# Performance work log

Hardware: AMD Instinct MI355X
Metric: run time of the kernel (lower is better)

## Reference

```python
import jax, jax.numpy as jnp
import numpy as np

WINDOW = 20  # local attention window, per create_sparse_mask


def _make_mask(rng, n, sparsity_ratio=0.1):
    # local band: |i - j| <= window//2 (covers start/end clamping and the diagonal)
    idx = jnp.arange(n)
    mask = jnp.abs(idx[:, None] - idx[None, :]) <= (WINDOW // 2)
    # random edges: n_random (i, j) pairs set to 1 (duplicates harmless)
    n_random = int(sparsity_ratio * n * n)
    k1, k2 = jax.random.split(rng)
    ri = jax.random.randint(k1, (n_random,), 0, n)
    rj = jax.random.randint(k2, (n_random,), 0, n)
    mask = mask.at[ri, rj].set(True)
    return mask  # [n, n] bool


def setup_inputs() -> dict:
    rng = jax.random.key(0)
    kq, kk, kv, km = jax.random.split(rng, 4)
    B, H, S, D = 1, 8, 4096, 32
    return {
        "query": jax.random.normal(kq, (B, H, S, D), dtype=jnp.float32),
        "key": jax.random.normal(kk, (B, H, S, D), dtype=jnp.float32),
        "value": jax.random.normal(kv, (B, H, S, D), dtype=jnp.float32),
        "mask": _make_mask(km, S, sparsity_ratio=0.1),
    }


def reference(query, key, value, mask):
    # query/key/value: [B, H, S, D]; mask: [S, S] bool (True = attend)
    head_dim = query.shape[-1]
    scale = 1.0 / jnp.sqrt(jnp.float32(head_dim))
    scores = jnp.einsum("bhqd,bhkd->bhqk", query, key) * scale
    # torch: scores = scores * mask; masked_fill(mask == 0, -inf) -> equivalent to where
    scores = jnp.where(mask[None, None, :, :], scores, -jnp.inf)
    attn = jax.nn.softmax(scores, axis=-1)
    attn = jnp.nan_to_num(attn, nan=0.0)
    return jnp.einsum("bhqk,bhkd->bhqd", attn, value)
```

## Files before the change

kernel.cpp:

```cpp
#include <hip/hip_runtime.h>
#include <hip/hip_bf16.h>


#define S_  4096
#define D_  32
#define H_  8

typedef _Float16 half8 __attribute__((ext_vector_type(8)));
typedef __fp16 fp16x2 __attribute__((ext_vector_type(2)));
typedef short short8 __attribute__((ext_vector_type(8)));
typedef short short4v __attribute__((ext_vector_type(4)));
typedef float float4v __attribute__((ext_vector_type(4)));
typedef unsigned short ushort_t;
typedef unsigned int u32;

#if __has_builtin(__builtin_amdgcn_exp2f)
#define EXP2(x) __builtin_amdgcn_exp2f(x)
#else
#define EXP2(x) exp2f(x)
#endif

#if __has_builtin(__builtin_amdgcn_sbfe)
#define SEXT_BIT(v, b) ((u32)__builtin_amdgcn_sbfe((int)(v), (b), 1))
#else
#define SEXT_BIT(v, b) ((u32)(((int)((v) << (31 - (b)))) >> 31))
#endif

__device__ inline ushort_t f2h(float x) {
    union { _Float16 h; ushort_t u; } c; c.h = (_Float16)x; return c.u;
}

__global__ __launch_bounds__(256)
void prep_all(const float* __restrict__ Q, const float* __restrict__ K,
              const float* __restrict__ V, const int* __restrict__ mask,
              ushort_t* __restrict__ Qh, ushort_t* __restrict__ Kt,
              ushort_t* __restrict__ Vt, ushort_t* __restrict__ mlane)
{
    __shared__ u32 msh[16 * 257];
    const int bx = blockIdx.x;
    const int tid = threadIdx.x;
    union U8 { ushort_t u[8]; short8 v; };

    if (bx < 512) {
        const int e0 = (bx * 256 + tid) * 8;
        const float c = 0.17677669529663687f * 1.4426950408889634f;
        float4 a = *(const float4*)(Q + e0);
        float4 b = *(const float4*)(Q + e0 + 4);
        float f[8] = {a.x*c, a.y*c, a.z*c, a.w*c, b.x*c, b.y*c, b.z*c, b.w*c};
        U8 o;
#pragma unroll
        for (int i = 0; i < 8; ++i) o.u[i] = f2h(f[i]);
        *(short8*)(Qh + e0) = o.v;
    } else if (bx < 1024) {
        const int e0 = ((bx - 512) * 256 + tid) * 8;
        const int n = (e0 >> 3) & 15, quad = (e0 >> 7) & 3, t16 = (e0 >> 9) & 3;
        const int kt = (e0 >> 11) & 63, h = e0 >> 17;
        const int krow = kt * 64 + t16 * 16 + n;
        const float* src = K + ((size_t)h * S_ + krow) * D_ + quad * 8;
        float4 a = *(const float4*)src;
        float4 b = *(const float4*)(src + 4);
        float f[8] = {a.x, a.y, a.z, a.w, b.x, b.y, b.z, b.w};
        U8 o;
#pragma unroll
        for (int i = 0; i < 8; ++i) o.u[i] = f2h(f[i]);
        *(short8*)(Kt + e0) = o.v;
    } else if (bx < 1536) {
        const int e0 = ((bx - 1024) * 256 + tid) * 8;
        const int n = (e0 >> 3) & 15, quad = (e0 >> 7) & 3;
        const int dhalf = (e0 >> 9) & 1, khalf = (e0 >> 10) & 1;
        const int kt = (e0 >> 11) & 63, h = e0 >> 17;
        const int d = dhalf * 16 + n;
        U8 o;
#pragma unroll
        for (int j = 0; j < 8; ++j) {
            int krow = kt * 64 + khalf * 32 + (j >> 2) * 16 + quad * 4 + (j & 3);
            o.u[j] = f2h(V[((size_t)h * S_ + krow) * D_ + d]);
        }
        *(short8*)(Vt + e0) = o.v;
    } else {
        const int mb = bx - 1536;
        const int qt16 = mb >> 2, cc = mb & 3;
#pragma unroll
        for (int i = 0; i < 16; ++i) {
            int4 m4 = *(const int4*)(mask + (size_t)(qt16 * 16 + i) * S_ + cc * 1024 + tid * 4);
            u32 v = (m4.x != 0 ? 1u : 0u) | (m4.y != 0 ? 0x100u : 0u)
                  | (m4.z != 0 ? 0x10000u : 0u) | (m4.w != 0 ? 0x1000000u : 0u);
            msh[i * 257 + tid] = v;
        }
        __syncthreads();
        const int kt_local = tid >> 4, g = tid & 15;
        const int qd = g >> 2, n4 = g & 3;
        u32 o16[4] = {0, 0, 0, 0};
#pragma unroll
        for (int t16 = 0; t16 < 4; ++t16) {
            const int cbase = kt_local * 16 + t16 * 4 + qd;
#pragma unroll
            for (int b = 0; b < 4; ++b) {
                u32 v = msh[(n4 * 4 + b) * 257 + cbase];
                u32 nib = ((v * 0x01020408u) >> 24) & 0xFu;
                o16[b] |= nib << (t16 * 4);
            }
        }
        union { u32 w2[2]; short4v s; } pk;
        pk.w2[0] = o16[0] | (o16[1] << 16);
        pk.w2[1] = o16[2] | (o16[3] << 16);
        const int kt = cc * 16 + kt_local;
        *(short4v*)(mlane + ((size_t)(qt16 * 64 + kt) * 64 + g * 4)) = pk.s;
    }
}


__device__ inline void gl_lds16(const ushort_t* g, ushort_t* l) {
    __builtin_amdgcn_global_load_lds((const __attribute__((address_space(1))) void*)g,
                                     (__attribute__((address_space(3))) void*)l,
                                     16, 0, 0);
}

__global__ __launch_bounds__(1024, 8)
void attn_mfma(const ushort_t* __restrict__ Qh, const ushort_t* __restrict__ Kt,
               const ushort_t* __restrict__ Vt, const ushort_t* __restrict__ mlane,
               float* __restrict__ out)
{
    __shared__ __align__(16) ushort_t sm[32768];
    ushort_t* K_s  = sm;
    ushort_t* Vt_s = sm + 16384;

    const int bid = blockIdx.x;
    const int swz = (bid & 7) * 64 + (bid >> 3);
    const int h  = swz >> 6;
    const int qb = swz & 63;
    const int q0 = qb * 64;

    const int tid = threadIdx.x;
    const int w = tid >> 6, l = tid & 63;
    const int kq = w >> 2, wl = w & 3;
    const int n16 = l & 15, quad = l >> 4;

    const int qt16_u = __builtin_amdgcn_readfirstlane(qb * 4 + wl);
    const ushort_t* mlw = mlane + ((size_t)qt16_u << 12);

    const int qrow = q0 + wl * 16 + n16;
    const half8 qh = *(const half8*)(Qh + ((size_t)h * S_ + qrow) * D_ + quad * 8);

    half8 ones;
#pragma unroll
    for (int i = 0; i < 8; ++i) ones[i] = (_Float16)1.0f;

    float4v o0 = {0.f, 0.f, 0.f, 0.f};
    float4v o1 = {0.f, 0.f, 0.f, 0.f};
    float4v lacc = {0.f, 0.f, 0.f, 0.f};

    const int gb = kq * 4096;
    const int kt_base = kq * 16;

    {
        const size_t tb = ((size_t)(h * 64 + kt_base)) * 2048 + wl * 512 + l * 8;
        gl_lds16(Kt + tb, K_s  + gb + wl * 512);
        gl_lds16(Vt + tb, Vt_s + gb + wl * 512);
    }
    __syncthreads();

    for (int i = 0; i < 16; ++i) {
        const int kt = kt_base + i;
        const int cb = gb + (i & 1) * 2048;
        if (i < 15) {
            const int nb = gb + ((i + 1) & 1) * 2048;
            const size_t tb = ((size_t)(h * 64 + kt + 1)) * 2048 + wl * 512 + l * 8;
            gl_lds16(Kt + tb, K_s  + nb + wl * 512);
            gl_lds16(Vt + tb, Vt_s + nb + wl * 512);
        }

        const u32 ml = mlw[kt * 64 + l];

        float pv[4][4];
#pragma unroll
        for (int t16 = 0; t16 < 4; ++t16) {
            const half8 kb = *(const half8*)(K_s + cb + (t16 * 4 + quad) * 128 + n16 * 8);
            float4v c = {0.f, 0.f, 0.f, 0.f};
            c = __builtin_amdgcn_mfma_f32_16x16x32_f16(kb, qh, c, 0, 0, 0);
#pragma unroll
            for (int r = 0; r < 4; ++r) {
                float e = EXP2(c[r]);
                u32 keep = SEXT_BIT(ml, t16 * 4 + r);
                pv[t16][r] = __uint_as_float(__float_as_uint(e) & keep);
            }
        }

#pragma unroll
        for (int kh = 0; kh < 2; ++kh) {
            union { fp16x2 hh[4]; half8 h8; } pk;
            pk.hh[0] = __builtin_amdgcn_cvt_pkrtz(pv[2*kh][0],   pv[2*kh][1]);
            pk.hh[1] = __builtin_amdgcn_cvt_pkrtz(pv[2*kh][2],   pv[2*kh][3]);
            pk.hh[2] = __builtin_amdgcn_cvt_pkrtz(pv[2*kh+1][0], pv[2*kh+1][1]);
            pk.hh[3] = __builtin_amdgcn_cvt_pkrtz(pv[2*kh+1][2], pv[2*kh+1][3]);
            const half8 pa = pk.h8;
            const half8 v0 = *(const half8*)(Vt_s + cb + ((kh * 2 + 0) * 4 + quad) * 128 + n16 * 8);
            const half8 v1 = *(const half8*)(Vt_s + cb + ((kh * 2 + 1) * 4 + quad) * 128 + n16 * 8);
            o0   = __builtin_amdgcn_mfma_f32_16x16x32_f16(pa, v0,   o0,   0, 0, 0);
            o1   = __builtin_amdgcn_mfma_f32_16x16x32_f16(pa, v1,   o1,   0, 0, 0);
            lacc = __builtin_amdgcn_mfma_f32_16x16x32_f16(pa, ones, lacc, 0, 0, 0);
        }

        __syncthreads();
    }

    float* red = (float*)sm;
    const int RSTR = 16 * 33 + 16;
    if (kq != 0) {
        float* ro = red + ((kq - 1) * 4 + wl) * RSTR;
#pragma unroll
        for (int reg = 0; reg < 4; ++reg) {
            const int r = quad * 4 + reg;
            ro[r * 33 + n16]      = o0[reg];
            ro[r * 33 + 16 + n16] = o1[reg];
            if (n16 == 0) ro[16 * 33 + r] = lacc[reg];
        }
    }
    __syncthreads();
    if (kq == 0) {
#pragma unroll
        for (int reg = 0; reg < 4; ++reg) {
            const int r = quad * 4 + reg;
            float s0 = o0[reg], s1 = o1[reg], sl = lacc[reg];
#pragma unroll
            for (int p = 0; p < 3; ++p) {
                const float* ro = red + (p * 4 + wl) * RSTR;
                s0 += ro[r * 33 + n16];
                s1 += ro[r * 33 + 16 + n16];
                sl += ro[16 * 33 + r];
            }
            const float inv = 1.0f / sl;
            const int row = q0 + wl * 16 + r;
            float* orow = out + ((size_t)h * S_ + row) * D_;
            orow[n16]      = s0 * inv;
            orow[16 + n16] = s1 * inv;
        }
    }
}


#define QT 64
#define KT 64
#define NSUB 4
#define KPT 16

__global__ __launch_bounds__(256, 2)
void sparse_attn_fp32(const float* __restrict__ Q, const float* __restrict__ K,
                      const float* __restrict__ V, const int* __restrict__ mask,
                      float* __restrict__ out)
{
    __shared__ float Ks[KT][D_];
    __shared__ float Vs[KT][D_];
    __shared__ float red_o[NSUB][QT][D_ + 1];
    __shared__ float red_l[NSUB][QT];

    const int h = blockIdx.y;
    const int q0 = blockIdx.x * QT;
    const int tid = threadIdx.x;
    const int ql = tid & 63;
    const int sub = tid >> 6;
    const int q = q0 + ql;
    const float scale = 0.17677669529663687f;

    float4 qreg[8];
    const float4* qrow = (const float4*)(Q + ((size_t)h * S_ + q) * D_);
#pragma unroll
    for (int i = 0; i < 8; ++i) qreg[i] = qrow[i];

    float o[D_];
#pragma unroll
    for (int d = 0; d < D_; ++d) o[d] = 0.f;
    float lsum0 = 0.f;

    const float* Kh = K + (size_t)h * S_ * D_;
    const float* Vh = V + (size_t)h * S_ * D_;

    for (int jt = 0; jt < S_; jt += KT) {
        __syncthreads();
        {
            const float4* gK = (const float4*)(Kh + (size_t)jt * D_);
            const float4* gV = (const float4*)(Vh + (size_t)jt * D_);
            float4* sK = (float4*)&Ks[0][0];
            float4* sV = (float4*)&Vs[0][0];
            sK[tid] = gK[tid]; sK[tid + 256] = gK[tid + 256];
            sV[tid] = gV[tid]; sV[tid + 256] = gV[tid + 256];
        }
        __syncthreads();

        int4 m4[4];
        {
            const int4* mr = (const int4*)(mask + (size_t)q * S_ + jt + sub * KPT);
#pragma unroll
            for (int i = 0; i < 4; ++i) m4[i] = mr[i];
        }
        const int* mb = (const int*)m4;

#pragma unroll
        for (int kk = 0; kk < KPT; ++kk) {
            const int jl = sub * KPT + kk;
            const float4* krow = (const float4*)&Ks[jl][0];
            float s = 0.f;
#pragma unroll
            for (int i = 0; i < 8; ++i) {
                float4 kv = krow[i];
                s += qreg[i].x * kv.x + qreg[i].y * kv.y + qreg[i].z * kv.z + qreg[i].w * kv.w;
            }
            const float p = mb[kk] ? __expf(s * scale) : 0.f;
            lsum0 += p;
            const float4* vrow = (const float4*)&Vs[jl][0];
#pragma unroll
            for (int i = 0; i < 8; ++i) {
                float4 vv = vrow[i];
                o[i * 4 + 0] += p * vv.x;
                o[i * 4 + 1] += p * vv.y;
                o[i * 4 + 2] += p * vv.z;
                o[i * 4 + 3] += p * vv.w;
            }
        }
    }

#pragma unroll
    for (int d = 0; d < D_; ++d) red_o[sub][ql][d] = o[d];
    red_l[sub][ql] = lsum0;
    __syncthreads();

    const int eq = tid & 63;
    const int dg = tid >> 6;
    float acc[8];
#pragma unroll
    for (int i = 0; i < 8; ++i) acc[i] = 0.f;
    float lsum = 0.f;
#pragma unroll
    for (int s2 = 0; s2 < NSUB; ++s2) {
        lsum += red_l[s2][eq];
#pragma unroll
        for (int i = 0; i < 8; ++i) acc[i] += red_o[s2][eq][dg * 8 + i];
    }
    const float inv = 1.0f / lsum;
    float* orow = out + ((size_t)h * S_ + q0 + eq) * D_ + dg * 8;
#pragma unroll
    for (int i = 0; i < 8; ++i) orow[i] = acc[i] * inv;
}


extern "C" void kernel_launch(void* const* d_in, const int* in_sizes, int n_in,
                              void* d_out, int out_size, void* d_ws, size_t ws_size,
                              hipStream_t stream) {
    const float* Q = (const float*)d_in[0];
    const float* K = (const float*)d_in[1];
    const float* V = (const float*)d_in[2];
    const int* mask = (const int*)d_in[3];
    float* out = (float*)d_out;

    const size_t MB = 1024 * 1024;
    if (ws_size < 8 * MB) {
        dim3 grid(S_ / QT, H_);
        sparse_attn_fp32<<<grid, 256, 0, stream>>>(Q, K, V, mask, out);
        return;
    }

    char* ws = (char*)d_ws;
    ushort_t* Qh = (ushort_t*)(ws + 0 * MB);
    ushort_t* Kt = (ushort_t*)(ws + 2 * MB);
    ushort_t* Vt = (ushort_t*)(ws + 4 * MB);
    ushort_t* mlane = (ushort_t*)(ws + 6 * MB);

    prep_all<<<2560, 256, 0, stream>>>(Q, K, V, mask, Qh, Kt, Vt, mlane);
    attn_mfma<<<512, 1024, 0, stream>>>(Qh, Kt, Vt, mlane, out);
}
```

Before: 139.7 us.

## Restructure attention kernel: per-wave 64-query tiles with direct global K/V loads

The block drops to 8 waves, and each wave handles all 64 query rows of the block (four 16-row subtiles held in registers) over its own slice of 8 key tiles. K and V fragments are now read straight from global memory instead of being staged through double-buffered LDS with global_load_lds, which removes the per-iteration __syncthreads. Each loaded K/V fragment is reused across four query subtiles. The cross-wave partial sums are combined with a three-stage tree reduction in LDS. The cost is higher register pressure from 12 accumulators per wave, uncoalesced global reads of K/V, and more reduction synchronisation at the end.

```diff
diff --git a/kernel.cpp b/kernel.cpp
--- a/kernel.cpp
+++ b/kernel.cpp
@@ -110,20 +110,13 @@
 }
 
 
-__device__ inline void gl_lds16(const ushort_t* g, ushort_t* l) {
-    __builtin_amdgcn_global_load_lds((const __attribute__((address_space(1))) void*)g,
-                                     (__attribute__((address_space(3))) void*)l,
-                                     16, 0, 0);
-}
-
-__global__ __launch_bounds__(1024, 8)
+__global__ __launch_bounds__(512, 4)
 void attn_mfma(const ushort_t* __restrict__ Qh, const ushort_t* __restrict__ Kt,
                const ushort_t* __restrict__ Vt, const ushort_t* __restrict__ mlane,
                float* __restrict__ out)
 {
-    __shared__ __align__(16) ushort_t sm[32768];
-    ushort_t* K_s  = sm;
-    ushort_t* Vt_s = sm + 16384;
+    __shared__ __align__(16) float red[4 * (64 * 33 + 64)];
+    const int RQ = 64 * 33 + 64;
 
     const int bid = blockIdx.x;
     const int swz = (bid & 7) * 64 + (bid >> 3);
@@ -133,109 +126,123 @@
 
     const int tid = threadIdx.x;
     const int w = tid >> 6, l = tid & 63;
-    const int kq = w >> 2, wl = w & 3;
     const int n16 = l & 15, quad = l >> 4;
 
-    const int qt16_u = __builtin_amdgcn_readfirstlane(qb * 4 + wl);
-    const ushort_t* mlw = mlane + ((size_t)qt16_u << 12);
-
-    const int qrow = q0 + wl * 16 + n16;
-    const half8 qh = *(const half8*)(Qh + ((size_t)h * S_ + qrow) * D_ + quad * 8);
+    const ushort_t* mlw = mlane + ((size_t)(qb * 4) << 12);
+
+    half8 qh[4];
+#pragma unroll
+    for (int qs = 0; qs < 4; ++qs)
+        qh[qs] = *(const half8*)(Qh + ((size_t)h * S_ + q0 + qs * 16 + n16) * D_ + quad * 8);
 
     half8 ones;
 #pragma unroll
     for (int i = 0; i < 8; ++i) ones[i] = (_Float16)1.0f;
 
-    float4v o0 = {0.f, 0.f, 0.f, 0.f};
-    float4v o1 = {0.f, 0.f, 0.f, 0.f};
-    float4v lacc = {0.f, 0.f, 0.f, 0.f};
-
-    const int gb = kq * 4096;
-    const int kt_base = kq * 16;
-
-    {
-        const size_t tb = ((size_t)(h * 64 + kt_base)) * 2048 + wl * 512 + l * 8;
-        gl_lds16(Kt + tb, K_s  + gb + wl * 512);
-        gl_lds16(Vt + tb, Vt_s + gb + wl * 512);
-    }
-    __syncthreads();
-
-    for (int i = 0; i < 16; ++i) {
-        const int kt = kt_base + i;
-        const int cb = gb + (i & 1) * 2048;
-        if (i < 15) {
-            const int nb = gb + ((i + 1) & 1) * 2048;
-            const size_t tb = ((size_t)(h * 64 + kt + 1)) * 2048 + wl * 512 + l * 8;
-            gl_lds16(Kt + tb, K_s  + nb + wl * 512);
-            gl_lds16(Vt + tb, Vt_s + nb + wl * 512);
-        }
-
-        const u32 ml = mlw[kt * 64 + l];
-
-        float pv[4][4];
-#pragma unroll
-        for (int t16 = 0; t16 < 4; ++t16) {
-            const half8 kb = *(const half8*)(K_s + cb + (t16 * 4 + quad) * 128 + n16 * 8);
-            float4v c = {0.f, 0.f, 0.f, 0.f};
-            c = __builtin_amdgcn_mfma_f32_16x16x32_f16(kb, qh, c, 0, 0, 0);
+    float4v o0[4], o1[4], lacc[4];
+#pragma unroll
+    for (int qs = 0; qs < 4; ++qs) {
+        o0[qs] = (float4v){0.f, 0.f, 0.f, 0.f};
+        o1[qs] = (float4v){0.f, 0.f, 0.f, 0.f};
+        lacc[qs] = (float4v){0.f, 0.f, 0.f, 0.f};
+    }
+
+    const int fo = quad * 128 + n16 * 8;
+    const ushort_t* Ktp = Kt + (size_t)h * 64 * 2048;
+    const ushort_t* Vtp = Vt + (size_t)h * 64 * 2048;
+
+    const int kt0 = w * 8;
+    for (int i = 0; i < 8; ++i) {
+        const int kt = kt0 + i;
+        const ushort_t* tb = Ktp + kt * 2048;
+        const ushort_t* vb = Vtp + kt * 2048;
+
+        u32 ml[4];
+#pragma unroll
+        for (int qs = 0; qs < 4; ++qs) ml[qs] = mlw[(qs << 12) + kt * 64 + l];
+
+#pragma unroll
+        for (int kh = 0; kh < 2; ++kh) {
+            const half8 kb0 = *(const half8*)(tb + kh * 1024 + fo);
+            const half8 kb1 = *(const half8*)(tb + kh * 1024 + 512 + fo);
+            const half8 v0  = *(const half8*)(vb + kh * 1024 + fo);
+            const half8 v1  = *(const half8*)(vb + kh * 1024 + 512 + fo);
+#pragma unroll
+            for (int qs = 0; qs < 4; ++qs) {
+                float4v c0 = {0.f, 0.f, 0.f, 0.f};
+                float4v c1 = {0.f, 0.f, 0.f, 0.f};
+                c0 = __builtin_amdgcn_mfma_f32_16x16x32_f16(kb0, qh[qs], c0, 0, 0, 0);
+                c1 = __builtin_amdgcn_mfma_f32_16x16x32_f16(kb1, qh[qs], c1, 0, 0, 0);
+                float f0[4], f1[4];
+#pragma unroll
+                for (int r = 0; r < 4; ++r) {
+                    float e0 = EXP2(c0[r]);
+                    float e1 = EXP2(c1[r]);
+                    u32 k0 = SEXT_BIT(ml[qs], kh * 8 + r);
+                    u32 k1 = SEXT_BIT(ml[qs], kh * 8 + 4 + r);
+                    f0[r] = __uint_as_float(__float_as_uint(e0) & k0);
+                    f1[r] = __uint_as_float(__float_as_uint(e1) & k1);
+                }
+                union { fp16x2 hh[4]; half8 h8; } pk;
+                pk.hh[0] = __builtin_amdgcn_cvt_pkrtz(f0[0], f0[1]);
+                pk.hh[1] = __builtin_amdgcn_cvt_pkrtz(f0[2], f0[3]);
+                pk.hh[2] = __builtin_amdgcn_cvt_pkrtz(f1[0], f1[1]);
+                pk.hh[3] = __builtin_amdgcn_cvt_pkrtz(f1[2], f1[3]);
+                const half8 pa = pk.h8;
+                o0[qs]   = __builtin_amdgcn_mfma_f32_16x16x32_f16(pa, v0,   o0[qs],   0, 0, 0);
+                o1[qs]   = __builtin_amdgcn_mfma_f32_16x16x32_f16(pa, v1,   o1[qs],   0, 0, 0);
+                lacc[qs] = __builtin_amdgcn_mfma_f32_16x16x32_f16(pa, ones, lacc[qs], 0, 0, 0);
+            }
+        }
+    }
+
+#define DUMP(slot) { \
+    float* ro = red + (slot) * RQ; \
+    _Pragma("unroll") for (int qs = 0; qs < 4; ++qs) \
+    _Pragma("unroll") for (int r = 0; r < 4; ++r) { \
+        const int q = qs * 16 + quad * 4 + r; \
+        ro[q * 33 + n16]      = o0[qs][r]; \
+        ro[q * 33 + 16 + n16] = o1[qs][r]; \
+        if (n16 == 0) ro[64 * 33 + q] = lacc[qs][r]; \
+    } }
+#define ADDIN(slot) { \
+    const float* ro = red + (slot) * RQ; \
+    _Pragma("unroll") for (int qs = 0; qs < 4; ++qs) \
+    _Pragma("unroll") for (int r = 0; r < 4; ++r) { \
+        const int q = qs * 16 + quad * 4 + r; \
+        o0[qs][r]   += ro[q * 33 + n16]; \
+        o1[qs][r]   += ro[q * 33 + 16 + n16]; \
+        lacc[qs][r] += ro[64 * 33 + q]; \
+    } }
+
+    if (w >= 4) DUMP(w - 4);
+    __syncthreads();
+    if (w < 4) ADDIN(w);
+    __syncthreads();
+    if (w == 2 || w == 3) DUMP(w - 2);
+    __syncthreads();
+    if (w < 2) ADDIN(w);
+    __syncthreads();
+    if (w == 1) DUMP(0);
+    __syncthreads();
+    if (w == 0) {
+        const float* ro = red + 0 * RQ;
+#pragma unroll
+        for (int qs = 0; qs < 4; ++qs)
 #pragma unroll
             for (int r = 0; r < 4; ++r) {
-                float e = EXP2(c[r]);
-                u32 keep = SEXT_BIT(ml, t16 * 4 + r);
-                pv[t16][r] = __uint_as_float(__float_as_uint(e) & keep);
-            }
-        }
-
-#pragma unroll
-        for (int kh = 0; kh < 2; ++kh) {
-            union { fp16x2 hh[4]; half8 h8; } pk;
-            pk.hh[0] = __builtin_amdgcn_cvt_pkrtz(pv[2*kh][0],   pv[2*kh][1]);
-            pk.hh[1] = __builtin_amdgcn_cvt_pkrtz(pv[2*kh][2],   pv[2*kh][3]);
-            pk.hh[2] = __builtin_amdgcn_cvt_pkrtz(pv[2*kh+1][0], pv[2*kh+1][1]);
-            pk.hh[3] = __builtin_amdgcn_cvt_pkrtz(pv[2*kh+1][2], pv[2*kh+1][3]);
-            const half8 pa = pk.h8;
-            const half8 v0 = *(const half8*)(Vt_s + cb + ((kh * 2 + 0) * 4 + quad) * 128 + n16 * 8);
-            const half8 v1 = *(const half8*)(Vt_s + cb + ((kh * 2 + 1) * 4 + quad) * 128 + n16 * 8);
-            o0   = __builtin_amdgcn_mfma_f32_16x16x32_f16(pa, v0,   o0,   0, 0, 0);
-            o1   = __builtin_amdgcn_mfma_f32_16x16x32_f16(pa, v1,   o1,   0, 0, 0);
-            lacc = __builtin_amdgcn_mfma_f32_16x16x32_f16(pa, ones, lacc, 0, 0, 0);
-        }
-
-        __syncthreads();
-    }
-
-    float* red = (float*)sm;
-    const int RSTR = 16 * 33 + 16;
-    if (kq != 0) {
-        float* ro = red + ((kq - 1) * 4 + wl) * RSTR;
-#pragma unroll
-        for (int reg = 0; reg < 4; ++reg) {
-            const int r = quad * 4 + reg;
-            ro[r * 33 + n16]      = o0[reg];
-            ro[r * 33 + 16 + n16] = o1[reg];
-            if (n16 == 0) ro[16 * 33 + r] = lacc[reg];
-        }
-    }
-    __syncthreads();
-    if (kq == 0) {
-#pragma unroll
-        for (int reg = 0; reg < 4; ++reg) {
-            const int r = quad * 4 + reg;
-            float s0 = o0[reg], s1 = o1[reg], sl = lacc[reg];
-#pragma unroll
-            for (int p = 0; p < 3; ++p) {
-                const float* ro = red + (p * 4 + wl) * RSTR;
-                s0 += ro[r * 33 + n16];
-                s1 += ro[r * 33 + 16 + n16];
-                sl += ro[16 * 33 + r];
-            }
-            const float inv = 1.0f / sl;
-            const int row = q0 + wl * 16 + r;
-            float* orow = out + ((size_t)h * S_ + row) * D_;
-            orow[n16]      = s0 * inv;
-            orow[16 + n16] = s1 * inv;
-        }
-    }
+                const int q = qs * 16 + quad * 4 + r;
+                const float s0 = o0[qs][r] + ro[q * 33 + n16];
+                const float s1 = o1[qs][r] + ro[q * 33 + 16 + n16];
+                const float sl = lacc[qs][r] + ro[64 * 33 + q];
+                const float inv = 1.0f / sl;
+                float* orow = out + ((size_t)h * S_ + q0 + q) * D_;
+                orow[n16]      = s0 * inv;
+                orow[16 + n16] = s1 * inv;
+            }
+    }
+#undef DUMP
+#undef ADDIN
 }
 
 
@@ -366,5 +373,5 @@
     ushort_t* mlane = (ushort_t*)(ws + 6 * MB);
 
     prep_all<<<2560, 256, 0, stream>>>(Q, K, V, mask, Qh, Kt, Vt, mlane);
-    attn_mfma<<<512, 1024, 0, stream>>>(Qh, Kt, Vt, mlane, out);
-}
+    attn_mfma<<<512, 512, 0, stream>>>(Qh, Kt, Vt, mlane, out);
+}
```

After: 140.7 us. No clear change (+0.7%).
